# Performance work log

Hardware: AMD Instinct MI355X
Metric: run time of the kernel (lower is better)

## Reference

```python
import jax, jax.numpy as jnp
import numpy as np

H = 64; W = 64; P = 16; NPH = 4; NPW = 4; PH = 16; PW = 16; ZD = 32; HD = 1024; UD = 3; B = 256


def affine_grid(theta, Ho, Wo):
    # torch F.affine_grid, align_corners=False. theta [N,2,3] -> grid [N,Ho,Wo,2]
    xs = (2.0 * jnp.arange(Wo, dtype=theta.dtype) + 1.0) / Wo - 1.0
    ys = (2.0 * jnp.arange(Ho, dtype=theta.dtype) + 1.0) / Ho - 1.0
    X, Y = jnp.meshgrid(xs, ys)  # [Ho,Wo] each, x varies along last axis
    base = jnp.stack([X, Y, jnp.ones_like(X)], axis=-1)  # [Ho,Wo,3]
    return jnp.einsum('nij,hwj->nhwi', theta, base)


def grid_sample(img, grid):
    # torch F.grid_sample bilinear, padding_mode='zeros', align_corners=False
    # img [N,H,W], grid [N,Ho,Wo,2] in [-1,1]
    Hi, Wi = img.shape[1], img.shape[2]
    x = (grid[..., 0] + 1.0) * Wi / 2.0 - 0.5
    y = (grid[..., 1] + 1.0) * Hi / 2.0 - 0.5
    x0 = jnp.floor(x); y0 = jnp.floor(y)
    wx = x - x0; wy = y - y0

    def gather(ix, iy):
        valid = (ix >= 0) & (ix < Wi) & (iy >= 0) & (iy < Hi)
        ixc = jnp.clip(ix, 0, Wi - 1).astype(jnp.int32)
        iyc = jnp.clip(iy, 0, Hi - 1).astype(jnp.int32)
        v = jax.vmap(lambda im, yy, xx: im[yy, xx])(img, iyc, ixc)
        return jnp.where(valid, v, 0.0)

    return (gather(x0, y0) * (1 - wx) * (1 - wy)
            + gather(x0 + 1, y0) * wx * (1 - wy)
            + gather(x0, y0 + 1) * (1 - wx) * wy
            + gather(x0 + 1, y0 + 1) * wx * wy)


def rot_tr(u):
    # rotTrMatrix: u [N,3] (angle, tx, ty) -> [N,2,3]
    c = jnp.cos(u[:, 0]); s = jnp.sin(u[:, 0])
    R = jnp.stack([jnp.stack([c, -s], -1), jnp.stack([s, c], -1)], -2)  # [N,2,2]
    return jnp.concatenate([R, u[:, 1:3, None]], axis=2)


def anchor_theta():
    # anchor_move: identity rotation + per-part grid-cell-center translations
    tx = (np.arange(NPW) * (W / NPW) + W / NPW / 2) / W - 0.5
    ty = (np.arange(NPH) * (H / NPH) + H / NPH / 2) / H - 0.5
    th = np.tile(np.concatenate([np.eye(2), np.zeros((2, 1))], axis=1)[None], (P, 1, 1)).astype(np.float32)
    for k in range(P):
        th[k, 0, 2] = tx[k % NPW]
        th[k, 1, 2] = ty[k // NPW]
    return jnp.asarray(th)


def forward(inputs, W1, b1, W2, b2, Wum, bum, Wuv, buv, Wgm, bgm, Wgv, bgv, Wz, M, eps_u, eps_g):
    hid = jax.nn.relu(inputs.reshape(-1, H * W) @ W1 + b1)
    hid = jax.nn.relu(hid @ W2 + b2)
    # global transform distribution (note: F.threshold(x,-6,6) -> 6 where x<=-6)
    gmu = jnp.tanh(hid @ Wgm + bgm)
    gpre = hid @ Wgv + bgv
    gvar = jnp.exp(jnp.where(gpre > -6.0, gpre, 6.0))
    gu = gmu + gvar * eps_g  # sample_u uses mu + var*eps (var, not std) as in source
    # per-part transform distribution (F.threshold(x,-6,-6) -> clamp below at -6)
    umu = jnp.tanh(hid @ Wum + bum)
    upre = hid @ Wuv + buv
    uvar = jnp.exp(jnp.where(upre > -6.0, upre, -6.0))
    u = (umu + uvar * eps_u).reshape(-1, UD)  # [B*P,3]
    # decode parts (input is ones, as in source)
    parts = jax.nn.sigmoid(jnp.ones((B, ZD), inputs.dtype) @ Wz).reshape(B * P, PH, PW)
    padh = (H - PH) // 2; padw = (W - PW) // 2
    parts = jnp.pad(parts, ((0, 0), (padh, H - PH - padh), (padw, W - PW - padw)))
    # anchor placement of parts and kernel masks
    th_a = jnp.tile(anchor_theta(), (B, 1, 1))  # [B*P,2,3], part-minor ordering
    g_a = affine_grid(th_a, H, W)
    parts = grid_sample(parts, g_a)                     # [B*P,H,W]
    KM = grid_sample(M[:B * P].reshape(B * P, H, W), g_a)
    # per-part rotation+translation for parts; translation-only for kernel
    theta = rot_tr(u)                                   # [B*P,2,3]
    g = affine_grid(theta, H, W)
    eye = jnp.broadcast_to(jnp.eye(2, dtype=theta.dtype), (B * P, 2, 2))
    theta_K = jnp.concatenate([eye, theta[:, :, 2:3]], axis=2)
    g_K = affine_grid(theta_K, H, W)
    KM = grid_sample(KM, g_K).reshape(B, P, H, W)
    xp = grid_sample(parts, g).reshape(B, P, H, W)
    # masked weighted compositing
    num = jnp.sum(xp * KM, axis=1)
    den = jnp.sum(KM, axis=1)
    den = jnp.where(den == 0.0, 1.0, den)
    x = num / den
    # global transform
    theta_g = rot_tr(gu)
    g_g = affine_grid(theta_g, H, W)
    return grid_sample(x, g_g)[:, None]  # [B,1,H,W]


def setup_inputs() -> dict:
    key = jax.random.key(0)
    ks = jax.random.split(key, 18)

    def lin(k, fin, fout):
        return jax.random.normal(k, (fin, fout), jnp.float32) / np.sqrt(fin)

    return {
        'inputs': jax.random.uniform(ks[0], (B, H * W), jnp.float32),
        'W1': lin(ks[1], H * W, HD), 'b1': jnp.zeros((HD,), jnp.float32),
        'W2': lin(ks[2], HD, HD), 'b2': jnp.zeros((HD,), jnp.float32),
        'Wum': lin(ks[3], HD, P * UD), 'bum': jnp.zeros((P * UD,), jnp.float32),
        'Wuv': lin(ks[4], HD, P * UD), 'buv': jnp.zeros((P * UD,), jnp.float32),
        'Wgm': lin(ks[5], HD, UD), 'bgm': jnp.zeros((UD,), jnp.float32),
        'Wgv': lin(ks[6], HD, UD), 'bgv': jnp.zeros((UD,), jnp.float32),
        'Wz': lin(ks[7], ZD, P * PH * PW),
        'M': jax.random.uniform(ks[8], (B * P, 1, H, W), jnp.float32),
        'eps_u': jax.random.normal(ks[9], (B, P * UD), jnp.float32),
        'eps_g': jax.random.normal(ks[10], (B, UD), jnp.float32),
    }


def reference(inputs, W1, b1, W2, b2, Wum, bum, Wuv, buv, Wgm, bgm, Wgv, bgv, Wz, M, eps_u, eps_g):
    return forward(inputs, W1, b1, W2, b2, Wum, bum, Wuv, buv, Wgm, bgm, Wgv, bgv, Wz, M, eps_u, eps_g)
```

## Files before the change

kernel.cpp:

```cpp
#include <hip/hip_runtime.h>
#include <math.h>

#define SPLITK 8
#define PSUM_STRIDE 262144

typedef __bf16 bf16x8 __attribute__((ext_vector_type(8)));
typedef float  f32x16 __attribute__((ext_vector_type(16)));

__device__ __forceinline__ unsigned short bf16rne(float x) {
    unsigned int u = __float_as_uint(x);
    unsigned int r = u + 0x7FFFu + ((u >> 16) & 1u);
    return (unsigned short)(r >> 16);
}
__device__ __forceinline__ float bf16tof(unsigned short h) {
    return __uint_as_float(((unsigned int)h) << 16);
}

__global__ __launch_bounds__(256) void prep_all(
    const float* __restrict__ inputs,
    const float* __restrict__ W1, const float* __restrict__ W2,
    const float* __restrict__ Wum, const float* __restrict__ Wuv,
    const float* __restrict__ Wgm, const float* __restrict__ Wgv,
    const float* __restrict__ Wz,
    unsigned short* __restrict__ Ahi, unsigned short* __restrict__ Alo,
    unsigned short* __restrict__ W1Thi, unsigned short* __restrict__ W1Tlo,
    unsigned short* __restrict__ W2Thi, unsigned short* __restrict__ W2Tlo,
    float* __restrict__ WT, float* __restrict__ partsb)
{
    __shared__ float t[32][33];
    int bid = blockIdx.x;
    int tid = threadIdx.x;
    if (bid < 4096 || (bid >= 5120 && bid < 6144)) {
        const float* W = (bid < 4096) ? W1 : W2;
        unsigned short* Thi = (bid < 4096) ? W1Thi : W2Thi;
        unsigned short* Tlo = (bid < 4096) ? W1Tlo : W2Tlo;
        int K = (bid < 4096) ? 4096 : 1024;
        int b2 = (bid < 4096) ? bid : (bid - 5120);
        int n0 = (b2 & 31) * 32, k0 = (b2 >> 5) * 32;
        int c = tid & 31, r0 = tid >> 5;
#pragma unroll
        for (int i = 0; i < 4; i++)
            t[r0 + 8 * i][c] = W[(size_t)(k0 + r0 + 8 * i) * 1024 + n0 + c];
        __syncthreads();
        int kk = tid & 31, n1 = tid >> 5;
#pragma unroll
        for (int i = 0; i < 4; i++) {
            float x = t[kk][n1 + 8 * i];
            unsigned short h = bf16rne(x);
            unsigned short l = bf16rne(x - bf16tof(h));
            size_t o = (size_t)(n0 + n1 + 8 * i) * K + k0 + kk;
            Thi[o] = h;
            Tlo[o] = l;
        }
    } else if (bid < 5120) {
        int id = ((bid - 4096) * 256 + tid) * 4;
        float4 x = *(const float4*)(inputs + id);
        ushort4 h, l;
        h.x = bf16rne(x.x); l.x = bf16rne(x.x - bf16tof(h.x));
        h.y = bf16rne(x.y); l.y = bf16rne(x.y - bf16tof(h.y));
        h.z = bf16rne(x.z); l.z = bf16rne(x.z - bf16tof(h.z));
        h.w = bf16rne(x.w); l.w = bf16rne(x.w - bf16tof(h.w));
        *(ushort4*)(Ahi + id) = h;
        *(ushort4*)(Alo + id) = l;
    } else if (bid < 6552) {
        int id = (bid - 6144) * 256 + tid;
        int o = id >> 10;
        int k = id & 1023;
        float v;
        if (o < 48)       v = Wum[k * 48 + o];
        else if (o < 96)  v = Wuv[k * 48 + (o - 48)];
        else if (o < 99)  v = Wgm[k * 3 + (o - 96)];
        else              v = Wgv[k * 3 + (o - 99)];
        WT[id] = v;
    } else {
        int idx = (bid - 6552) * 256 + tid;
        float s = 0.f;
#pragma unroll
        for (int z = 0; z < 32; z++) s += Wz[z * 4096 + idx];
        partsb[idx] = 1.f / (1.f + expf(-s));
    }
}

__global__ __launch_bounds__(256) void gemm_bf16x3(
    const unsigned short* __restrict__ Ahi, const unsigned short* __restrict__ Alo,
    const unsigned short* __restrict__ Bhi, const unsigned short* __restrict__ Blo,
    float* __restrict__ psum, int K, int kchunk)
{
    __shared__ unsigned short Ah[4096], Al[4096], Bh[4096], Bl[4096];
    int tid = threadIdx.x;
    int n0 = blockIdx.x * 64, m0 = blockIdx.y * 64;
    int kb = blockIdx.z * kchunk;
    int wid = tid >> 6, lane = tid & 63;
    int wm = wid & 1, wn = wid >> 1;
    int lr = lane & 31, hi = lane >> 5;

    int r0 = tid >> 3, ch0 = tid & 7;
    int r1 = (tid + 256) >> 3, ch1 = (tid + 256) & 7;
    int l0 = r0 * 64 + 8 * (ch0 ^ (r0 & 7));
    int l1 = r1 * 64 + 8 * (ch1 ^ (r1 & 7));
    size_t ga0 = (size_t)(m0 + r0) * K + kb + ch0 * 8;
    size_t ga1 = (size_t)(m0 + r1) * K + kb + ch1 * 8;
    size_t gb0 = (size_t)(n0 + r0) * K + kb + ch0 * 8;
    size_t gb1 = (size_t)(n0 + r1) * K + kb + ch1 * 8;

    f32x16 acc_hh = {}, acc_hl = {}, acc_lh = {};

    int nkt = kchunk >> 6;
    uint4 vah0, vah1, val0, val1, vbh0, vbh1, vbl0, vbl1;
    vah0 = *(const uint4*)(Ahi + ga0);
    vah1 = *(const uint4*)(Ahi + ga1);
    val0 = *(const uint4*)(Alo + ga0);
    val1 = *(const uint4*)(Alo + ga1);
    vbh0 = *(const uint4*)(Bhi + gb0);
    vbh1 = *(const uint4*)(Bhi + gb1);
    vbl0 = *(const uint4*)(Blo + gb0);
    vbl1 = *(const uint4*)(Blo + gb1);

    int basea = (wm * 32 + lr) * 64;
    int baseb = (wn * 32 + lr) * 64;
    int sw = lr & 7;

    for (int kt = 0; kt < nkt; kt++) {
        __syncthreads();
        *(uint4*)(Ah + l0) = vah0;
        *(uint4*)(Ah + l1) = vah1;
        *(uint4*)(Al + l0) = val0;
        *(uint4*)(Al + l1) = val1;
        *(uint4*)(Bh + l0) = vbh0;
        *(uint4*)(Bh + l1) = vbh1;
        *(uint4*)(Bl + l0) = vbl0;
        *(uint4*)(Bl + l1) = vbl1;
        __syncthreads();
        if (kt + 1 < nkt) {
            size_t o = (size_t)(kt + 1) * 64;
            vah0 = *(const uint4*)(Ahi + ga0 + o);
            vah1 = *(const uint4*)(Ahi + ga1 + o);
            val0 = *(const uint4*)(Alo + ga0 + o);
            val1 = *(const uint4*)(Alo + ga1 + o);
            vbh0 = *(const uint4*)(Bhi + gb0 + o);
            vbh1 = *(const uint4*)(Bhi + gb1 + o);
            vbl0 = *(const uint4*)(Blo + gb0 + o);
            vbl1 = *(const uint4*)(Blo + gb1 + o);
        }
#pragma unroll
        for (int s = 0; s < 4; s++) {
            int cidx = 8 * (((s << 1) + hi) ^ sw);
            bf16x8 afh = *(const bf16x8*)(Ah + basea + cidx);
            bf16x8 afl = *(const bf16x8*)(Al + basea + cidx);
            bf16x8 bfh = *(const bf16x8*)(Bh + baseb + cidx);
            bf16x8 bfl = *(const bf16x8*)(Bl + baseb + cidx);
            acc_hh = __builtin_amdgcn_mfma_f32_32x32x16_bf16(afh, bfh, acc_hh, 0, 0, 0);
            acc_hl = __builtin_amdgcn_mfma_f32_32x32x16_bf16(afh, bfl, acc_hl, 0, 0, 0);
            acc_lh = __builtin_amdgcn_mfma_f32_32x32x16_bf16(afl, bfh, acc_lh, 0, 0, 0);
        }
    }

    float* op = psum + (size_t)blockIdx.z * PSUM_STRIDE;
    int colg = n0 + wn * 32 + lr;
#pragma unroll
    for (int r = 0; r < 16; r++) {
        int rowl = (r & 3) + 8 * (r >> 2) + 4 * hi;
        op[(size_t)(m0 + wm * 32 + rowl) * 1024 + colg] = acc_hh[r] + acc_hl[r] + acc_lh[r];
    }
}

__global__ __launch_bounds__(256) void reduce_bias_relu_split(
    const float* __restrict__ psum, const float* __restrict__ bias,
    unsigned short* __restrict__ hi, unsigned short* __restrict__ lo)
{
    int i = (blockIdx.x * 256 + threadIdx.x) * 4;
    float4 v = *(const float4*)(psum + i);
#pragma unroll
    for (int s = 1; s < SPLITK; s++) {
        float4 t = *(const float4*)(psum + (size_t)s * PSUM_STRIDE + i);
        v.x += t.x; v.y += t.y; v.z += t.z; v.w += t.w;
    }
    float4 bb = *(const float4*)(bias + (i & 1023));
    v.x = fmaxf(v.x + bb.x, 0.f);
    v.y = fmaxf(v.y + bb.y, 0.f);
    v.z = fmaxf(v.z + bb.z, 0.f);
    v.w = fmaxf(v.w + bb.w, 0.f);
    ushort4 h, l;
    h.x = bf16rne(v.x); l.x = bf16rne(v.x - bf16tof(h.x));
    h.y = bf16rne(v.y); l.y = bf16rne(v.y - bf16tof(h.y));
    h.z = bf16rne(v.z); l.z = bf16rne(v.z - bf16tof(h.z));
    h.w = bf16rne(v.w); l.w = bf16rne(v.w - bf16tof(h.w));
    *(ushort4*)(hi + i) = h;
    *(ushort4*)(lo + i) = l;
}

__global__ __launch_bounds__(1024) void composite_heads(
    const float* __restrict__ psum, const float* __restrict__ b2,
    const float* __restrict__ WT,
    const float* __restrict__ bum, const float* __restrict__ buv,
    const float* __restrict__ bgm, const float* __restrict__ bgv,
    const float* __restrict__ eps_u, const float* __restrict__ eps_g,
    const float* __restrict__ M, const float* __restrict__ parts,
    float* __restrict__ out)
{
    __shared__ float patch[4096];
    __shared__ float planes[8][4096];
    __shared__ float h2[1024];
    __shared__ float u_raw[51];
    __shared__ float pc[16], psn[16], ptx[16], pty[16], pwx[16], pwy[16];
    __shared__ int pix[16], piy[16];
    int b = blockIdx.x;
    int tid = threadIdx.x;

    const float* Mb = M + ((size_t)(b * 16) << 12);

    float4 st[8];
#pragma unroll
    for (int q = 0; q < 8; q++)
        st[q] = ((const float4*)(Mb + (size_t)q * 4096))[tid];

    {
        float v = psum[(size_t)b * 1024 + tid];
#pragma unroll
        for (int s = 1; s < SPLITK; s++)
            v += psum[(size_t)s * PSUM_STRIDE + (size_t)b * 1024 + tid];
        h2[tid] = fmaxf(v + b2[tid], 0.f);
    }
    for (int i = tid; i < 4096; i += 1024) patch[i] = parts[i];
    __syncthreads();

    {
        int w = tid >> 6, l = tid & 63;
        const float4* h4 = (const float4*)h2;
        float4 hr0 = h4[l], hr1 = h4[64 + l], hr2 = h4[128 + l], hr3 = h4[192 + l];
        for (int o = w; o < 51; o += 16) {
            int rm = (o < 48) ? o : (48 + o);
            int rv = (o < 48) ? (o + 48) : (51 + o);
            const float* wpm = WT + rm * 1024 + l * 4;
            const float* wpv = WT + rv * 1024 + l * 4;
            float4 wm0 = *(const float4*)(wpm);
            float4 wm1 = *(const float4*)(wpm + 256);
            float4 wm2 = *(const float4*)(wpm + 512);
            float4 wm3 = *(const float4*)(wpm + 768);
            float4 wv0 = *(const float4*)(wpv);
            float4 wv1 = *(const float4*)(wpv + 256);
            float4 wv2 = *(const float4*)(wpv + 512);
            float4 wv3 = *(const float4*)(wpv + 768);
            float am = 0.f, av = 0.f;
            am = fmaf(hr0.x, wm0.x, am); am = fmaf(hr0.y, wm0.y, am);
            am = fmaf(hr0.z, wm0.z, am); am = fmaf(hr0.w, wm0.w, am);
            av = fmaf(hr0.x, wv0.x, av); av = fmaf(hr0.y, wv0.y, av);
            av = fmaf(hr0.z, wv0.z, av); av = fmaf(hr0.w, wv0.w, av);
            am = fmaf(hr1.x, wm1.x, am); am = fmaf(hr1.y, wm1.y, am);
            am = fmaf(hr1.z, wm1.z, am); am = fmaf(hr1.w, wm1.w, am);
            av = fmaf(hr1.x, wv1.x, av); av = fmaf(hr1.y, wv1.y, av);
            av = fmaf(hr1.z, wv1.z, av); av = fmaf(hr1.w, wv1.w, av);
            am = fmaf(hr2.x, wm2.x, am); am = fmaf(hr2.y, wm2.y, am);
            am = fmaf(hr2.z, wm2.z, am); am = fmaf(hr2.w, wm2.w, am);
            av = fmaf(hr2.x, wv2.x, av); av = fmaf(hr2.y, wv2.y, av);
            av = fmaf(hr2.z, wv2.z, av); av = fmaf(hr2.w, wv2.w, av);
            am = fmaf(hr3.x, wm3.x, am); am = fmaf(hr3.y, wm3.y, am);
            am = fmaf(hr3.z, wm3.z, am); am = fmaf(hr3.w, wm3.w, am);
            av = fmaf(hr3.x, wv3.x, av); av = fmaf(hr3.y, wv3.y, av);
            av = fmaf(hr3.z, wv3.z, av); av = fmaf(hr3.w, wv3.w, av);
#pragma unroll
            for (int s = 32; s; s >>= 1) {
                am += __shfl_xor(am, s, 64);
                av += __shfl_xor(av, s, 64);
            }
            if (l == 0) {
                if (o < 48) {
                    float umu = tanhf(am + bum[o]);
                    float uvar = expf(fmaxf(av + buv[o], -6.f));
                    u_raw[o] = umu + uvar * eps_u[b * 48 + o];
                } else {
                    int n = o - 48;
                    float gmu = tanhf(am + bgm[n]);
                    float gpre = av + bgv[n];
                    float gvar = expf(gpre > -6.f ? gpre : 6.f);
                    u_raw[o] = gmu + gvar * eps_g[b * 3 + n];
                }
            }
        }
    }
    __syncthreads();

    if (tid < 16) {
        float ang = u_raw[tid * 3 + 0];
        float tx = u_raw[tid * 3 + 1], ty = u_raw[tid * 3 + 2];
        pc[tid] = cosf(ang);
        psn[tid] = sinf(ang);
        ptx[tid] = tx;
        pty[tid] = ty;
        float ax = fminf(fmaxf(32.f * tx, -16384.f), 16384.f);
        float fax = floorf(ax);
        pwx[tid] = ax - fax;
        pix[tid] = (int)fax;
        float ay = fminf(fmaxf(32.f * ty, -16384.f), 16384.f);
        float fay = floorf(ay);
        pwy[tid] = ay - fay;
        piy[tid] = (int)fay;
    }

#pragma unroll
    for (int q = 0; q < 8; q++) ((float4*)planes[q])[tid] = st[q];
#pragma unroll
    for (int q = 0; q < 8; q++)
        st[q] = ((const float4*)(Mb + (size_t)(8 + q) * 4096))[tid];
    __syncthreads();

    int j = tid & 63;
    int i0 = (tid >> 6) * 4;
    float xnv = (float)(2 * j + 1) * (1.f / 64.f) - 1.f;
    float ynv0 = (float)(2 * i0 + 1) * (1.f / 64.f) - 1.f;

    float num[4] = {}, den[4] = {};

#define COMP_PART(p) do {                                                     \
        int dx = 8 * ((p) & 3) - 12;                                          \
        int dy = 8 * ((p) >> 2) - 12;                                         \
        float c = pc[p], s = psn[p], tx = ptx[p], ty = pty[p];                \
        float wx = pwx[p], wy = pwy[p];                                       \
        int ix = pix[p], iy = piy[p];                                         \
        int iY = iy + dy;                                                     \
        int x0 = j + ix;                                                      \
        int X = x0 + dx;                                                      \
        bool vc0 = ((unsigned)x0 < 64u) && ((unsigned)X < 64u);               \
        bool vc1 = ((unsigned)(x0 + 1) < 64u) && ((unsigned)(X + 1) < 64u);   \
        float w0 = vc0 ? (1.f - wx) : 0.f;                                    \
        float w1 = vc1 ? wx : 0.f;                                            \
        int Xc0 = min(max(X, 0), 63);                                         \
        int Xc1 = min(max(X + 1, 0), 63);                                     \
        const float* pl = planes[(p) & 7];                                    \
        float R[5];                                                           \
        _Pragma("unroll")                                                     \
        for (int r = 0; r < 5; r++) {                                         \
            int i = i0 + r;                                                   \
            int ri = i + iY;                                                  \
            bool vr = ((unsigned)(i + iy) < 64u) && ((unsigned)ri < 64u);     \
            int ric = min(max(ri, 0), 63);                                    \
            const float* row = pl + (ric << 6);                               \
            float val = fmaf(w0, row[Xc0], w1 * row[Xc1]);                    \
            R[r] = vr ? val : 0.f;                                            \
        }                                                                     \
        float gx0 = fmaf(-s, ynv0, fmaf(c, xnv, tx));                         \
        float gy0 = fmaf(c, ynv0, fmaf(s, xnv, ty));                          \
        float xs = fmaf(gx0, 32.f, 31.5f);                                    \
        float ysv = fmaf(gy0, 32.f, 31.5f);                                   \
        int ox = 24 - dx, oy = 24 - dy;                                       \
        float oxf = (float)ox, oyf = (float)oy;                               \
        const float* pp = patch + ((p) << 8);                                 \
        _Pragma("unroll")                                                     \
        for (int r = 0; r < 4; r++) {                                         \
            float km = fmaf(wy, R[r + 1] - R[r], R[r]);                       \
            den[r] += km;                                                     \
            if (xs >= oxf - 1.f && xs < oxf + 16.f &&                         \
                ysv >= oyf - 1.f && ysv < oyf + 16.f) {                       \
                float xf = floorf(xs), yf = floorf(ysv);                      \
                float wxx = xs - xf, wyy = ysv - yf;                          \
                int a0 = (int)yf - oy;                                        \
                int b0c = (int)xf - ox;                                       \
                float v00 = 0.f, v10 = 0.f, v01 = 0.f, v11 = 0.f;             \
                if ((unsigned)a0 < 16u) {                                     \
                    const float* pr = pp + a0 * 16;                           \
                    if ((unsigned)b0c < 16u) v00 = pr[b0c];                   \
                    if ((unsigned)(b0c + 1) < 16u) v10 = pr[b0c + 1];         \
                }                                                             \
                if ((unsigned)(a0 + 1) < 16u) {                               \
                    const float* pr = pp + (a0 + 1) * 16;                     \
                    if ((unsigned)b0c < 16u) v01 = pr[b0c];                   \
                    if ((unsigned)(b0c + 1) < 16u) v11 = pr[b0c + 1];         \
                }                                                             \
                float top = fmaf(wxx, v10 - v00, v00);                        \
                float bot = fmaf(wxx, v11 - v01, v01);                        \
                float xp = fmaf(wyy, bot - top, top);                         \
                num[r] = fmaf(xp, km, num[r]);                                \
            }                                                                 \
            xs -= s;                                                          \
            ysv += c;                                                         \
        }                                                                     \
    } while (0)

#pragma unroll
    for (int p = 0; p < 8; p++) COMP_PART(p);

    __syncthreads();
#pragma unroll
    for (int q = 0; q < 8; q++) ((float4*)planes[q])[tid] = st[q];
    __syncthreads();

#pragma unroll
    for (int p = 8; p < 16; p++) COMP_PART(p);
#undef COMP_PART

    __syncthreads();
    float* xl = planes[0];
#pragma unroll
    for (int r = 0; r < 4; r++) {
        float d = (den[r] == 0.f) ? 1.f : den[r];
        xl[(i0 + r) * 64 + j] = num[r] / d;
    }
    __syncthreads();

    float ang = u_raw[48], gtx = u_raw[49], gty = u_raw[50];
    float cg = cosf(ang), sg = sinf(ang);
    float* ob = out + ((size_t)b << 12);
#pragma unroll
    for (int r = 0; r < 4; r++) {
        int i = i0 + r;
        float ynv = (float)(2 * i + 1) * (1.f / 64.f) - 1.f;
        float gx = cg * xnv - sg * ynv + gtx;
        float gy = sg * xnv + cg * ynv + gty;
        gx = fminf(fmaxf(gx, -8.f), 8.f);
        gy = fminf(fmaxf(gy, -8.f), 8.f);
        float xs = fmaf(gx, 32.f, 31.5f);
        float ysv = fmaf(gy, 32.f, 31.5f);
        float xf = floorf(xs), yf = floorf(ysv);
        float wx = xs - xf, wy = ysv - yf;
        int x0 = (int)xf, y0 = (int)yf;
        float v00 = 0.f, v10 = 0.f, v01 = 0.f, v11 = 0.f;
        bool vx0 = (unsigned)x0 < 64u, vx1 = (unsigned)(x0 + 1) < 64u;
        if ((unsigned)y0 < 64u) {
            const float* row = xl + y0 * 64;
            if (vx0) v00 = row[x0];
            if (vx1) v10 = row[x0 + 1];
        }
        if ((unsigned)(y0 + 1) < 64u) {
            const float* row = xl + (y0 + 1) * 64;
            if (vx0) v01 = row[x0];
            if (vx1) v11 = row[x0 + 1];
        }
        float top = fmaf(wx, v10 - v00, v00);
        float bot = fmaf(wx, v11 - v01, v01);
        ob[i * 64 + j] = fmaf(wy, bot - top, top);
    }
}

extern "C" void kernel_launch(void* const* d_in, const int* in_sizes, int n_in,
                              void* d_out, int out_size, void* d_ws, size_t ws_size,
                              hipStream_t stream)
{
    (void)in_sizes; (void)n_in; (void)out_size; (void)ws_size;
    const float* inputs = (const float*)d_in[0];
    const float* W1  = (const float*)d_in[1];
    const float* b1  = (const float*)d_in[2];
    const float* W2  = (const float*)d_in[3];
    const float* b2  = (const float*)d_in[4];
    const float* Wum = (const float*)d_in[5];
    const float* bum = (const float*)d_in[6];
    const float* Wuv = (const float*)d_in[7];
    const float* buv = (const float*)d_in[8];
    const float* Wgm = (const float*)d_in[9];
    const float* bgm = (const float*)d_in[10];
    const float* Wgv = (const float*)d_in[11];
    const float* bgv = (const float*)d_in[12];
    const float* Wz  = (const float*)d_in[13];
    const float* Mm  = (const float*)d_in[14];
    const float* eps_u = (const float*)d_in[15];
    const float* eps_g = (const float*)d_in[16];

    float* ws = (float*)d_ws;
    float* psum      = ws;
    float* parts_buf = psum + 8 * PSUM_STRIDE;
    float* WTh_buf   = parts_buf + 4096;
    unsigned short* us = (unsigned short*)(WTh_buf + 104448);
    unsigned short* Ahi   = us;
    unsigned short* Alo   = Ahi + 1048576;
    unsigned short* W1Thi = Alo + 1048576;
    unsigned short* W1Tlo = W1Thi + 4194304;
    unsigned short* W2Thi = W1Tlo + 4194304;
    unsigned short* W2Tlo = W2Thi + 1048576;
    unsigned short* H1hi  = W2Tlo + 1048576;
    unsigned short* H1lo  = H1hi + 262144;

    prep_all<<<6568, 256, 0, stream>>>(inputs, W1, W2, Wum, Wuv, Wgm, Wgv, Wz,
                                       Ahi, Alo, W1Thi, W1Tlo, W2Thi, W2Tlo,
                                       WTh_buf, parts_buf);

    gemm_bf16x3<<<dim3(16, 4, SPLITK), 256, 0, stream>>>(Ahi, Alo, W1Thi, W1Tlo,
                                                         psum, 4096, 4096 / SPLITK);
    reduce_bias_relu_split<<<256, 256, 0, stream>>>(psum, b1, H1hi, H1lo);
    gemm_bf16x3<<<dim3(16, 4, SPLITK), 256, 0, stream>>>(H1hi, H1lo, W2Thi, W2Tlo,
                                                         psum, 1024, 1024 / SPLITK);
    composite_heads<<<256, 1024, 0, stream>>>(psum, b2, WTh_buf, bum, buv,
                                              bgm, bgv, eps_u, eps_g,
                                              Mm, parts_buf, (float*)d_out);
}
```

Measured before the change: 222.9 us.

## Double-buffer mask planes via direct global-to-LDS loads in composite kernel

```diff
diff --git a/kernel.cpp b/kernel.cpp
--- a/kernel.cpp
+++ b/kernel.cpp
@@ -14,6 +14,13 @@
 }
 __device__ __forceinline__ float bf16tof(unsigned short h) {
     return __uint_as_float(((unsigned int)h) << 16);
+}
+
+__device__ __forceinline__ void stage16(const float* g, float* ldsWaveBase) {
+    __builtin_amdgcn_global_load_lds(
+        (const __attribute__((address_space(1))) unsigned int*)g,
+        (__attribute__((address_space(3))) unsigned int*)ldsWaveBase,
+        16, 0, 0);
 }
 
 __global__ __launch_bounds__(256) void prep_all(
@@ -199,20 +206,21 @@
     float* __restrict__ out)
 {
     __shared__ float patch[4096];
-    __shared__ float planes[8][4096];
+    __shared__ float bufA[4][4096];
+    __shared__ float bufB[4][4096];
     __shared__ float h2[1024];
     __shared__ float u_raw[51];
     __shared__ float pc[16], psn[16], ptx[16], pty[16], pwx[16], pwy[16];
     __shared__ int pix[16], piy[16];
     int b = blockIdx.x;
     int tid = threadIdx.x;
+    int wbase = (tid >> 6) * 256;
 
     const float* Mb = M + ((size_t)(b * 16) << 12);
 
-    float4 st[8];
-#pragma unroll
-    for (int q = 0; q < 8; q++)
-        st[q] = ((const float4*)(Mb + (size_t)q * 4096))[tid];
+#pragma unroll
+    for (int q = 0; q < 4; q++)
+        stage16(Mb + (size_t)q * 4096 + tid * 4, &bufA[q][wbase]);
 
     {
         float v = psum[(size_t)b * 1024 + tid];
@@ -223,6 +231,10 @@
     }
     for (int i = tid; i < 4096; i += 1024) patch[i] = parts[i];
     __syncthreads();
+
+#pragma unroll
+    for (int q = 0; q < 4; q++)
+        stage16(Mb + (size_t)(4 + q) * 4096 + tid * 4, &bufB[q][wbase]);
 
     {
         int w = tid >> 6, l = tid & 63;
@@ -296,12 +308,6 @@
         pwy[tid] = ay - fay;
         piy[tid] = (int)fay;
     }
-
-#pragma unroll
-    for (int q = 0; q < 8; q++) ((float4*)planes[q])[tid] = st[q];
-#pragma unroll
-    for (int q = 0; q < 8; q++)
-        st[q] = ((const float4*)(Mb + (size_t)(8 + q) * 4096))[tid];
     __syncthreads();
 
     int j = tid & 63;
@@ -311,7 +317,7 @@
 
     float num[4] = {}, den[4] = {};
 
-#define COMP_PART(p) do {                                                     \
+#define COMP_PART(p, BUF) do {                                                \
         int dx = 8 * ((p) & 3) - 12;                                          \
         int dy = 8 * ((p) >> 2) - 12;                                         \
         float c = pc[p], s = psn[p], tx = ptx[p], ty = pty[p];                \
@@ -326,7 +332,7 @@
         float w1 = vc1 ? wx : 0.f;                                            \
         int Xc0 = min(max(X, 0), 63);                                         \
         int Xc1 = min(max(X + 1, 0), 63);                                     \
-        const float* pl = planes[(p) & 7];                                    \
+        const float* pl = BUF[(p) & 3];                                       \
         float R[5];                                                           \
         _Pragma("unroll")                                                     \
         for (int r = 0; r < 5; r++) {                                         \
@@ -377,19 +383,34 @@
     } while (0)
 
 #pragma unroll
-    for (int p = 0; p < 8; p++) COMP_PART(p);
-
-    __syncthreads();
-#pragma unroll
-    for (int q = 0; q < 8; q++) ((float4*)planes[q])[tid] = st[q];
-    __syncthreads();
-
-#pragma unroll
-    for (int p = 8; p < 16; p++) COMP_PART(p);
+    for (int p = 0; p < 4; p++) COMP_PART(p, bufA);
+
+    __syncthreads();
+#pragma unroll
+    for (int q = 0; q < 4; q++)
+        stage16(Mb + (size_t)(8 + q) * 4096 + tid * 4, &bufA[q][wbase]);
+
+#pragma unroll
+    for (int p = 4; p < 8; p++) COMP_PART(p, bufB);
+
+    asm volatile("s_waitcnt vmcnt(0)" ::: "memory");
+    __syncthreads();
+#pragma unroll
+    for (int q = 0; q < 4; q++)
+        stage16(Mb + (size_t)(12 + q) * 4096 + tid * 4, &bufB[q][wbase]);
+
+#pragma unroll
+    for (int p = 8; p < 12; p++) COMP_PART(p, bufA);
+
+    asm volatile("s_waitcnt vmcnt(0)" ::: "memory");
+    __syncthreads();
+
+#pragma unroll
+    for (int p = 12; p < 16; p++) COMP_PART(p, bufB);
 #undef COMP_PART
 
     __syncthreads();
-    float* xl = planes[0];
+    float* xl = bufA[0];
 #pragma unroll
     for (int r = 0; r < 4; r++) {
         float d = (den[r] == 0.f) ? 1.f : den[r];
```

Measured after the change: 196.1 us. -12.0%, faster.
